# Kernel optimization log

Hardware: AMD Instinct MI355X
Metric: run time of the kernel (lower is better)

Reference implementation:

```python
import jax, jax.numpy as jnp
import numpy as np

BLOCK_SIZE = 256
N_EMBD = 384
HEAD_SIZE = 384
B = 256
T = 256


def setup_inputs() -> dict:
    key = jax.random.key(0)
    kx, kk, kq, kv = jax.random.split(key, 4)
    scale = 1.0 / np.sqrt(N_EMBD)
    x = jax.random.normal(kx, (B, T, N_EMBD), dtype=jnp.float32)
    Wk = jax.random.normal(kk, (HEAD_SIZE, N_EMBD), dtype=jnp.float32) * scale
    Wq = jax.random.normal(kq, (HEAD_SIZE, N_EMBD), dtype=jnp.float32) * scale
    Wv = jax.random.normal(kv, (HEAD_SIZE, N_EMBD), dtype=jnp.float32) * scale
    return {"x": x, "Wk": Wk, "Wq": Wq, "Wv": Wv}


def reference(x, Wk, Wq, Wv):
    # Single-head causal self-attention; equals forward_with_cache at prefill
    # (fresh cache, cache_index=0, T tokens) and forward_no_cache.
    # Linear layers are bias-free: y = x @ W.T
    k = jnp.einsum('btc,hc->bth', x, Wk)  # [B,T,H]
    q = jnp.einsum('btc,hc->bth', x, Wq)
    v = jnp.einsum('btc,hc->bth', x, Wv)
    inv_sqrt_hs = jnp.asarray(HEAD_SIZE, x.dtype) ** -0.5
    wei = jnp.einsum('bth,bsh->bts', q, k) * inv_sqrt_hs  # [B,T,T]
    causal = jnp.tril(jnp.ones((T, T), dtype=bool))
    wei = jnp.where(causal, wei, jnp.asarray(-jnp.inf, wei.dtype))
    wei = jax.nn.softmax(wei, axis=-1)
    # dropout is identity in eval mode
    out = jnp.einsum('bts,bsh->bth', wei, v)  # [B,T,H]
    return out
```

## Files before the change

### kernel.cpp

```cpp
#include <hip/hip_runtime.h>

#define B_ 256
#define T_ 256
#define C_ 384
#define H_ 384

typedef float f4 __attribute__((ext_vector_type(4)));
typedef float f32x4 __attribute__((ext_vector_type(4)));
typedef short bf8 __attribute__((ext_vector_type(8)));
typedef short s8v __attribute__((ext_vector_type(8)));
typedef short s4v __attribute__((ext_vector_type(4)));

__device__ __forceinline__ short f2bf(float f) {
  unsigned u = __builtin_bit_cast(unsigned, f);
  u += 0x7FFFu + ((u >> 16) & 1u);
  return (short)(u >> 16);
}

__device__ __forceinline__ void gload_lds16(const void* g, void* l) {
  __builtin_amdgcn_global_load_lds(
      (const __attribute__((address_space(1))) unsigned int*)g,
      (__attribute__((address_space(3))) unsigned int*)l, 16, 0, 0);
}

__global__ __launch_bounds__(256) void convert_kernel(
    const float* __restrict__ x, const float* __restrict__ wk,
    const float* __restrict__ wq, const float* __restrict__ wv,
    short* __restrict__ xb, short* __restrict__ wb) {
  const int NXG = (B_ * T_ * C_) / 8;
  const int NWG = (H_ * C_) / 8;
  const int total = NXG + 3 * NWG;
  for (int g = blockIdx.x * 256 + threadIdx.x; g < total; g += gridDim.x * 256) {
    const float* src;
    short* dst;
    if (g < NXG) {
      src = x + (size_t)g * 8;
      dst = xb + (size_t)g * 8;
    } else {
      int h = g - NXG;
      int wsel = h / NWG;
      int o = h - wsel * NWG;
      const float* wp = wsel == 0 ? wk : (wsel == 1 ? wq : wv);
      src = wp + (size_t)o * 8;
      dst = wb + (size_t)wsel * (H_ * C_) + (size_t)o * 8;
    }
    f4 f0 = *(const f4*)src;
    f4 f1 = *(const f4*)(src + 4);
    s8v r;
    r[0] = f2bf(f0[0]); r[1] = f2bf(f0[1]); r[2] = f2bf(f0[2]); r[3] = f2bf(f0[3]);
    r[4] = f2bf(f1[0]); r[5] = f2bf(f1[1]); r[6] = f2bf(f1[2]); r[7] = f2bf(f1[3]);
    *(s8v*)dst = r;
  }
}

__global__ __launch_bounds__(512, 2) void proj_gemm(
    const short* __restrict__ xb, const short* __restrict__ wb,
    short* __restrict__ kb, short* __restrict__ qbuf, short* __restrict__ vt) {
  __shared__ __align__(16) short lA[2][512 * 64];
  __shared__ __align__(16) short lB[2][128 * 64];
  const int tid = threadIdx.x;
  const int bid = blockIdx.x;
  const int swz = (bid & 7) * 144 + (bid >> 3);
  const int nb = swz % 9;
  const int mb = swz / 9;
  const int m0 = mb * 512, gn0 = nb * 128;
  const int w = tid >> 6, l = tid & 63;
  const int wrm = w >> 1, wcn = w & 1;

  auto STAGE = [&](int buf, int t) {
    const int k0 = t * 64;
#pragma unroll
    for (int j = 0; j < 8; ++j) {
      const int flat = j * 512 + tid;
      const int row = flat >> 3;
      const int colg = ((flat & 7) ^ (row & 7)) * 8;
      gload_lds16(xb + (size_t)(m0 + row) * C_ + k0 + colg,
                  (char*)&lA[buf][0] + flat * 16);
    }
#pragma unroll
    for (int j = 0; j < 2; ++j) {
      const int flat = j * 512 + tid;
      const int row = flat >> 3;
      const int colg = ((flat & 7) ^ (row & 7)) * 8;
      gload_lds16(wb + (size_t)(gn0 + row) * C_ + k0 + colg,
                  (char*)&lB[buf][0] + flat * 16);
    }
  };

  f32x4 acc[8][4] = {};
  STAGE(0, 0);
#pragma unroll
  for (int t = 0; t < 6; ++t) {
    const int cur = t & 1;
    if (t < 5) {
      STAGE(cur ^ 1, t + 1);
      asm volatile("s_waitcnt vmcnt(10)" ::: "memory");
    } else {
      asm volatile("s_waitcnt vmcnt(0)" ::: "memory");
    }
    __builtin_amdgcn_s_barrier();
    __builtin_amdgcn_sched_barrier(0);
    const short* A = &lA[cur][0];
    const short* Bt = &lB[cur][0];
#pragma unroll
    for (int ks = 0; ks < 2; ++ks) {
      const int kg = ks * 4 + (l >> 4);
      bf8 av[8], bv[4];
#pragma unroll
      for (int mt = 0; mt < 8; ++mt) {
        const int ra = wrm * 128 + mt * 16 + (l & 15);
        av[mt] = *(const bf8*)&A[ra * 64 + ((kg ^ (ra & 7)) << 3)];
      }
#pragma unroll
      for (int nt = 0; nt < 4; ++nt) {
        const int rb = wcn * 64 + nt * 16 + (l & 15);
        bv[nt] = *(const bf8*)&Bt[rb * 64 + ((kg ^ (rb & 7)) << 3)];
      }
      __builtin_amdgcn_s_setprio(1);
#pragma unroll
      for (int mt = 0; mt < 8; ++mt)
#pragma unroll
        for (int nt = 0; nt < 4; ++nt)
          acc[mt][nt] = __builtin_amdgcn_mfma_f32_16x16x32_bf16(
              av[mt], bv[nt], acc[mt][nt], 0, 0, 0);
      __builtin_amdgcn_s_setprio(0);
    }
    __builtin_amdgcn_sched_barrier(0);
    __builtin_amdgcn_s_barrier();
  }
  const int proj = nb / 3;
  const int gcb = (nb % 3) * 128 + wcn * 64 + (l & 15);
  const int tok0 = m0 + wrm * 128 + ((l >> 4) * 4);
  if (proj < 2) {
    short* dst = proj == 0 ? kb : qbuf;
#pragma unroll
    for (int mt = 0; mt < 8; ++mt)
#pragma unroll
      for (int nt = 0; nt < 4; ++nt)
#pragma unroll
        for (int r = 0; r < 4; ++r)
          dst[(size_t)(tok0 + mt * 16 + r) * H_ + gcb + nt * 16] =
              f2bf(acc[mt][nt][r]);
  } else {
    const int bb = tok0 >> 8;
    const int tl0 = tok0 & 255;
#pragma unroll
    for (int mt = 0; mt < 8; ++mt)
#pragma unroll
      for (int nt = 0; nt < 4; ++nt) {
        s4v pk;
        pk[0] = f2bf(acc[mt][nt][0]); pk[1] = f2bf(acc[mt][nt][1]);
        pk[2] = f2bf(acc[mt][nt][2]); pk[3] = f2bf(acc[mt][nt][3]);
        *(s4v*)&vt[(size_t)bb * (H_ * T_) + (size_t)(gcb + nt * 16) * T_ +
                   tl0 + mt * 16] = pk;
      }
  }
}

__global__ __launch_bounds__(256, 2) void attn_kernel(
    const short* __restrict__ qbuf, const short* __restrict__ kb,
    const short* __restrict__ vt, float* __restrict__ out) {
  __shared__ __align__(16) short Kl[2][256 * 64];
  short* Pl = &Kl[0][0];
  const int bid = blockIdx.x;
  const int swzb = (bid & 7) * 128 + (bid >> 3);
  const int b = swzb >> 2;
  const int qi = swzb & 3;
  const int t0 = qi * 64;
  const int SKV = t0 + 64;
  const int ntile = SKV >> 4;
  const int nks = SKV >> 5;
  const int tid = threadIdx.x;
  const int w = tid >> 6, l = tid & 63;

  bf8 qv[6][2];
  {
    const short* qrow =
        qbuf + (size_t)(b * T_ + t0 + w * 16 + (l & 15)) * H_ + (l >> 4) * 8;
#pragma unroll
    for (int hc = 0; hc < 6; ++hc)
#pragma unroll
      for (int ks = 0; ks < 2; ++ks)
        qv[hc][ks] = *(const bf8*)(qrow + hc * 64 + ks * 32);
  }

  auto STAGE = [&](int buf, int hc) {
    const int h0 = hc * 64;
#pragma unroll
    for (int j = 0; j < 8; ++j) {
      const int flat = j * 256 + tid;
      const int row = flat >> 3;
      const int colg = ((flat & 7) ^ (row & 7)) * 8;
      gload_lds16(kb + (size_t)(b * T_ + row) * H_ + h0 + colg,
                  (char*)&Kl[buf][0] + flat * 16);
    }
  };

  f32x4 sa[16] = {};
  STAGE(0, 0);
#pragma unroll
  for (int hc = 0; hc < 6; ++hc) {
    if (hc < 5) {
      STAGE((hc + 1) & 1, hc + 1);
      asm volatile("s_waitcnt vmcnt(8)" ::: "memory");
    } else {
      asm volatile("s_waitcnt vmcnt(0)" ::: "memory");
    }
    __builtin_amdgcn_s_barrier();
    __builtin_amdgcn_sched_barrier(0);
    const short* Kb = &Kl[hc & 1][0];
#pragma unroll
    for (int ks = 0; ks < 2; ++ks) {
      const int kg = ks * 4 + (l >> 4);
      __builtin_amdgcn_s_setprio(1);
#pragma unroll
      for (int nt = 0; nt < 16; ++nt)
        if (nt < ntile) {
          const int rk = nt * 16 + (l & 15);
          bf8 bv = *(const bf8*)&Kb[rk * 64 + ((kg ^ (rk & 7)) << 3)];
          sa[nt] = __builtin_amdgcn_mfma_f32_16x16x32_bf16(qv[hc][ks], bv,
                                                           sa[nt], 0, 0, 0);
        }
      __builtin_amdgcn_s_setprio(0);
    }
    __builtin_amdgcn_sched_barrier(0);
    __builtin_amdgcn_s_barrier();
  }

  const float scale = 0.05103103630798287f;
  const int rbl = w * 16 + (l >> 4) * 4;
#pragma unroll
  for (int r = 0; r < 4; ++r) {
    const int prow = rbl + r;
    const int trow = t0 + prow;
    float vv[16];
    float m = -3.0e38f;
#pragma unroll
    for (int nt = 0; nt < 16; ++nt)
      if (nt < ntile) {
        const int col = nt * 16 + (l & 15);
        float v = sa[nt][r] * scale;
        if (col > trow) v = -3.0e38f;
        vv[nt] = v;
        m = fmaxf(m, v);
      }
    m = fmaxf(m, __shfl_xor(m, 1));
    m = fmaxf(m, __shfl_xor(m, 2));
    m = fmaxf(m, __shfl_xor(m, 4));
    m = fmaxf(m, __shfl_xor(m, 8));
    float s = 0.f;
#pragma unroll
    for (int nt = 0; nt < 16; ++nt)
      if (nt < ntile) {
        vv[nt] = __expf(vv[nt] - m);
        s += vv[nt];
      }
    s += __shfl_xor(s, 1);
    s += __shfl_xor(s, 2);
    s += __shfl_xor(s, 4);
    s += __shfl_xor(s, 8);
    const float inv = 1.0f / s;
    const int sw = (prow & 7) << 3;
#pragma unroll
    for (int nt = 0; nt < 16; ++nt)
      if (nt < ntile) {
        const int col = nt * 16 + (l & 15);
        Pl[prow * 256 + (col ^ sw)] = f2bf(vv[nt] * inv);
      }
  }
  __syncthreads();

  const size_t vbase = (size_t)b * (H_ * T_);
  bf8 vc[6], vn[6];
  {
    const int kk0 = (l >> 4) * 8;
#pragma unroll
    for (int nt = 0; nt < 6; ++nt)
      vc[nt] = *(const bf8*)&vt[vbase + (size_t)(w * 96 + nt * 16 + (l & 15)) * T_ + kk0];
  }
  f32x4 o[4][6] = {};
  for (int ks = 0; ks < nks; ++ks) {
    const int kk = ks * 32 + (l >> 4) * 8;
    if (ks + 1 < nks) {
      const int kk2 = kk + 32;
#pragma unroll
      for (int nt = 0; nt < 6; ++nt)
        vn[nt] = *(const bf8*)&vt[vbase + (size_t)(w * 96 + nt * 16 + (l & 15)) * T_ + kk2];
    }
    bf8 av[4];
#pragma unroll
    for (int mt = 0; mt < 4; ++mt) {
      const int rp = mt * 16 + (l & 15);
      av[mt] = *(const bf8*)&Pl[rp * 256 + (kk ^ ((rp & 7) << 3))];
    }
    __builtin_amdgcn_s_setprio(1);
#pragma unroll
    for (int nt = 0; nt < 6; ++nt)
#pragma unroll
      for (int mt = 0; mt < 4; ++mt)
        o[mt][nt] = __builtin_amdgcn_mfma_f32_16x16x32_bf16(av[mt], vc[nt],
                                                            o[mt][nt], 0, 0, 0);
    __builtin_amdgcn_s_setprio(0);
#pragma unroll
    for (int nt = 0; nt < 6; ++nt) vc[nt] = vn[nt];
  }
#pragma unroll
  for (int mt = 0; mt < 4; ++mt) {
    const int tok = b * T_ + t0 + mt * 16 + (l >> 4) * 4;
#pragma unroll
    for (int nt = 0; nt < 6; ++nt) {
      const int d = w * 96 + nt * 16 + (l & 15);
#pragma unroll
      for (int r = 0; r < 4; ++r)
        out[(size_t)(tok + r) * H_ + d] = o[mt][nt][r];
    }
  }
}

extern "C" void kernel_launch(void* const* d_in, const int* in_sizes, int n_in,
                              void* d_out, int out_size, void* d_ws, size_t ws_size,
                              hipStream_t stream) {
  (void)in_sizes; (void)n_in; (void)out_size; (void)ws_size;
  const float* x = (const float*)d_in[0];
  const float* wk = (const float*)d_in[1];
  const float* wq = (const float*)d_in[2];
  const float* wv = (const float*)d_in[3];
  float* out = (float*)d_out;
  char* ws = (char*)d_ws;
  const size_t SZ = (size_t)B_ * T_ * H_ * 2;
  short* kbuf = (short*)ws;
  short* qbuf = (short*)(ws + SZ);
  short* vt   = (short*)(ws + 2 * SZ);
  short* xb = (short*)d_out;
  short* wb = (short*)((char*)d_out + SZ);
  convert_kernel<<<2048, 256, 0, stream>>>(x, wk, wq, wv, xb, wb);
  proj_gemm<<<1152, 512, 0, stream>>>(xb, wb, kbuf, qbuf, vt);
  attn_kernel<<<1024, 256, 0, stream>>>(qbuf, kbuf, vt, out);
}
```

Baseline: 326.2 us.

## Fuse fp32-to-bf16 conversion into projection GEMM tile loading

Drops the separate convert kernel. The projection GEMM now reads fp32 x and weights straight from global memory into registers, packs them to bf16 with v_cvt_pk_bf16_f32, and writes them into LDS. This removes a full write and re-read of a bf16 copy of x plus one kernel launch. In exchange it gives up async global_load_lds in favour of register staging, which raises register pressure, and each of the 9 N-blocks rereads fp32 x, doubling the bytes per reread.

```diff
diff --git a/kernel.cpp b/kernel.cpp
--- a/kernel.cpp
+++ b/kernel.cpp
@@ -8,8 +8,8 @@
 typedef float f4 __attribute__((ext_vector_type(4)));
 typedef float f32x4 __attribute__((ext_vector_type(4)));
 typedef short bf8 __attribute__((ext_vector_type(8)));
-typedef short s8v __attribute__((ext_vector_type(8)));
 typedef short s4v __attribute__((ext_vector_type(4)));
+typedef unsigned int u4v __attribute__((ext_vector_type(4)));
 
 __device__ __forceinline__ short f2bf(float f) {
   unsigned u = __builtin_bit_cast(unsigned, f);
@@ -17,44 +17,30 @@
   return (short)(u >> 16);
 }
 
+__device__ __forceinline__ unsigned cvtpk(float a, float b) {
+  unsigned r;
+  asm("v_cvt_pk_bf16_f32 %0, %1, %2" : "=v"(r) : "v"(a), "v"(b));
+  return r;
+}
+
+__device__ __forceinline__ u4v pack8(f4 lo, f4 hi) {
+  u4v r;
+  r[0] = cvtpk(lo[0], lo[1]);
+  r[1] = cvtpk(lo[2], lo[3]);
+  r[2] = cvtpk(hi[0], hi[1]);
+  r[3] = cvtpk(hi[2], hi[3]);
+  return r;
+}
+
 __device__ __forceinline__ void gload_lds16(const void* g, void* l) {
   __builtin_amdgcn_global_load_lds(
       (const __attribute__((address_space(1))) unsigned int*)g,
       (__attribute__((address_space(3))) unsigned int*)l, 16, 0, 0);
 }
 
-__global__ __launch_bounds__(256) void convert_kernel(
+__global__ __launch_bounds__(512, 2) void proj_gemm(
     const float* __restrict__ x, const float* __restrict__ wk,
     const float* __restrict__ wq, const float* __restrict__ wv,
-    short* __restrict__ xb, short* __restrict__ wb) {
-  const int NXG = (B_ * T_ * C_) / 8;
-  const int NWG = (H_ * C_) / 8;
-  const int total = NXG + 3 * NWG;
-  for (int g = blockIdx.x * 256 + threadIdx.x; g < total; g += gridDim.x * 256) {
-    const float* src;
-    short* dst;
-    if (g < NXG) {
-      src = x + (size_t)g * 8;
-      dst = xb + (size_t)g * 8;
-    } else {
-      int h = g - NXG;
-      int wsel = h / NWG;
-      int o = h - wsel * NWG;
-      const float* wp = wsel == 0 ? wk : (wsel == 1 ? wq : wv);
-      src = wp + (size_t)o * 8;
-      dst = wb + (size_t)wsel * (H_ * C_) + (size_t)o * 8;
-    }
-    f4 f0 = *(const f4*)src;
-    f4 f1 = *(const f4*)(src + 4);
-    s8v r;
-    r[0] = f2bf(f0[0]); r[1] = f2bf(f0[1]); r[2] = f2bf(f0[2]); r[3] = f2bf(f0[3]);
-    r[4] = f2bf(f1[0]); r[5] = f2bf(f1[1]); r[6] = f2bf(f1[2]); r[7] = f2bf(f1[3]);
-    *(s8v*)dst = r;
-  }
-}
-
-__global__ __launch_bounds__(512, 2) void proj_gemm(
-    const short* __restrict__ xb, const short* __restrict__ wb,
     short* __restrict__ kb, short* __restrict__ qbuf, short* __restrict__ vt) {
   __shared__ __align__(16) short lA[2][512 * 64];
   __shared__ __align__(16) short lB[2][128 * 64];
@@ -63,43 +49,60 @@
   const int swz = (bid & 7) * 144 + (bid >> 3);
   const int nb = swz % 9;
   const int mb = swz / 9;
-  const int m0 = mb * 512, gn0 = nb * 128;
+  const int m0 = mb * 512;
   const int w = tid >> 6, l = tid & 63;
   const int wrm = w >> 1, wcn = w & 1;
-
-  auto STAGE = [&](int buf, int t) {
+  const int proj = nb / 3;
+  const float* Wp = proj == 0 ? wk : (proj == 1 ? wq : wv);
+  const int wrow0 = (nb % 3) * 128;
+
+  f4 ar[8][2];
+  f4 br[2][2];
+
+  auto LOADT = [&](int t) {
     const int k0 = t * 64;
 #pragma unroll
     for (int j = 0; j < 8; ++j) {
       const int flat = j * 512 + tid;
       const int row = flat >> 3;
-      const int colg = ((flat & 7) ^ (row & 7)) * 8;
-      gload_lds16(xb + (size_t)(m0 + row) * C_ + k0 + colg,
-                  (char*)&lA[buf][0] + flat * 16);
+      const int cg = ((flat & 7) ^ (row & 7)) * 8;
+      const float* p = x + (size_t)(m0 + row) * C_ + k0 + cg;
+      ar[j][0] = *(const f4*)p;
+      ar[j][1] = *(const f4*)(p + 4);
     }
 #pragma unroll
     for (int j = 0; j < 2; ++j) {
       const int flat = j * 512 + tid;
       const int row = flat >> 3;
-      const int colg = ((flat & 7) ^ (row & 7)) * 8;
-      gload_lds16(wb + (size_t)(gn0 + row) * C_ + k0 + colg,
-                  (char*)&lB[buf][0] + flat * 16);
+      const int cg = ((flat & 7) ^ (row & 7)) * 8;
+      const float* p = Wp + (size_t)(wrow0 + row) * C_ + k0 + cg;
+      br[j][0] = *(const f4*)p;
+      br[j][1] = *(const f4*)(p + 4);
     }
   };
+  auto WRITET = [&](int buf) {
+#pragma unroll
+    for (int j = 0; j < 8; ++j) {
+      const int flat = j * 512 + tid;
+      *(u4v*)((char*)&lA[buf][0] + flat * 16) = pack8(ar[j][0], ar[j][1]);
+    }
+#pragma unroll
+    for (int j = 0; j < 2; ++j) {
+      const int flat = j * 512 + tid;
+      *(u4v*)((char*)&lB[buf][0] + flat * 16) = pack8(br[j][0], br[j][1]);
+    }
+  };
 
   f32x4 acc[8][4] = {};
-  STAGE(0, 0);
+  LOADT(0);
+  WRITET(0);
+  asm volatile("s_waitcnt lgkmcnt(0)" ::: "memory");
+  __builtin_amdgcn_s_barrier();
+  __builtin_amdgcn_sched_barrier(0);
 #pragma unroll
   for (int t = 0; t < 6; ++t) {
     const int cur = t & 1;
-    if (t < 5) {
-      STAGE(cur ^ 1, t + 1);
-      asm volatile("s_waitcnt vmcnt(10)" ::: "memory");
-    } else {
-      asm volatile("s_waitcnt vmcnt(0)" ::: "memory");
-    }
-    __builtin_amdgcn_s_barrier();
-    __builtin_amdgcn_sched_barrier(0);
+    if (t < 5) LOADT(t + 1);
     const short* A = &lA[cur][0];
     const short* Bt = &lB[cur][0];
 #pragma unroll
@@ -125,10 +128,12 @@
               av[mt], bv[nt], acc[mt][nt], 0, 0, 0);
       __builtin_amdgcn_s_setprio(0);
     }
+    if (t < 5) WRITET(cur ^ 1);
+    asm volatile("s_waitcnt lgkmcnt(0)" ::: "memory");
     __builtin_amdgcn_sched_barrier(0);
     __builtin_amdgcn_s_barrier();
-  }
-  const int proj = nb / 3;
+    __builtin_amdgcn_sched_barrier(0);
+  }
   const int gcb = (nb % 3) * 128 + wcn * 64 + (l & 15);
   const int tok0 = m0 + wrm * 128 + ((l >> 4) * 4);
   if (proj < 2) {
@@ -331,9 +336,6 @@
   short* kbuf = (short*)ws;
   short* qbuf = (short*)(ws + SZ);
   short* vt   = (short*)(ws + 2 * SZ);
-  short* xb = (short*)d_out;
-  short* wb = (short*)((char*)d_out + SZ);
-  convert_kernel<<<2048, 256, 0, stream>>>(x, wk, wq, wv, xb, wb);
-  proj_gemm<<<1152, 512, 0, stream>>>(xb, wb, kbuf, qbuf, vt);
+  proj_gemm<<<1152, 512, 0, stream>>>(x, wk, wq, wv, kbuf, qbuf, vt);
   attn_kernel<<<1024, 256, 0, stream>>>(qbuf, kbuf, vt, out);
 }
```

Result: slower. 610.0 us (+87.0%).

## Keep weight tile resident in LDS and stream four 128-row A tiles per block

Applied to the files above, without the earlier changes.

The projection GEMM now loads the block's full 128x384 weight slice into LDS once and keeps it there. It then streams four consecutive 128-row x tiles through a 4-deep LDS ring buffer, writing each output tile as soon as its K loop finishes. Blocks shrink to 256 threads with smaller per-wave accumulators and one block per CU, which removes repeated weight loads. The cost is lower occupancy, a large LDS footprint, and epilogue stores that now sit inside the main loop.

```diff
diff --git a/kernel.cpp b/kernel.cpp
--- a/kernel.cpp
+++ b/kernel.cpp
@@ -53,72 +53,72 @@
   }
 }
 
-__global__ __launch_bounds__(512, 2) void proj_gemm(
+__global__ __launch_bounds__(256, 1) void proj_gemm(
     const short* __restrict__ xb, const short* __restrict__ wb,
     short* __restrict__ kb, short* __restrict__ qbuf, short* __restrict__ vt) {
-  __shared__ __align__(16) short lA[2][512 * 64];
-  __shared__ __align__(16) short lB[2][128 * 64];
+  __shared__ __align__(16) short Bres[128 * 384];
+  __shared__ __align__(16) short Abuf[4][128 * 64];
   const int tid = threadIdx.x;
   const int bid = blockIdx.x;
   const int swz = (bid & 7) * 144 + (bid >> 3);
   const int nb = swz % 9;
-  const int mb = swz / 9;
-  const int m0 = mb * 512, gn0 = nb * 128;
+  const int mg = swz / 9;
+  const int gn0 = nb * 128;
   const int w = tid >> 6, l = tid & 63;
-  const int wrm = w >> 1, wcn = w & 1;
-
-  auto STAGE = [&](int buf, int t) {
-    const int k0 = t * 64;
-#pragma unroll
-    for (int j = 0; j < 8; ++j) {
-      const int flat = j * 512 + tid;
-      const int row = flat >> 3;
-      const int colg = ((flat & 7) ^ (row & 7)) * 8;
-      gload_lds16(xb + (size_t)(m0 + row) * C_ + k0 + colg,
-                  (char*)&lA[buf][0] + flat * 16);
-    }
-#pragma unroll
-    for (int j = 0; j < 2; ++j) {
-      const int flat = j * 512 + tid;
-      const int row = flat >> 3;
-      const int colg = ((flat & 7) ^ (row & 7)) * 8;
-      gload_lds16(wb + (size_t)(gn0 + row) * C_ + k0 + colg,
-                  (char*)&lB[buf][0] + flat * 16);
+  const int wr = w >> 1, wc = w & 1;
+
+#pragma unroll
+  for (int j = 0; j < 24; ++j) {
+    const int flat = j * 256 + tid;
+    const int row = flat / 48;
+    const int g = flat % 48;
+    const int kc = g >> 3, sub = g & 7;
+    const int colg = kc * 64 + ((sub ^ (row & 7)) << 3);
+    gload_lds16(wb + (size_t)(gn0 + row) * C_ + colg, (char*)Bres + flat * 16);
+  }
+  auto SA = [&](int i) {
+    const int m0 = (mg * 4 + i / 6) * 128;
+    const int k0 = (i % 6) * 64;
+    char* dst = (char*)&Abuf[i & 3][0];
+#pragma unroll
+    for (int j = 0; j < 4; ++j) {
+      const int flat = j * 256 + tid;
+      const int row = flat >> 3, sub = flat & 7;
+      const int colg = (sub ^ (row & 7)) << 3;
+      gload_lds16(xb + (size_t)(m0 + row) * C_ + k0 + colg, dst + flat * 16);
     }
   };
 
-  f32x4 acc[8][4] = {};
-  STAGE(0, 0);
-#pragma unroll
-  for (int t = 0; t < 6; ++t) {
-    const int cur = t & 1;
-    if (t < 5) {
-      STAGE(cur ^ 1, t + 1);
-      asm volatile("s_waitcnt vmcnt(10)" ::: "memory");
-    } else {
-      asm volatile("s_waitcnt vmcnt(0)" ::: "memory");
-    }
+  SA(0); SA(1); SA(2);
+  f32x4 acc[4][4] = {};
+#pragma unroll
+  for (int i = 0; i < 24; ++i) {
+    if (i + 3 < 24) SA(i + 3);
+    if (i <= 20)      asm volatile("s_waitcnt vmcnt(12)" ::: "memory");
+    else if (i == 21) asm volatile("s_waitcnt vmcnt(8)" ::: "memory");
+    else if (i == 22) asm volatile("s_waitcnt vmcnt(4)" ::: "memory");
+    else              asm volatile("s_waitcnt vmcnt(0)" ::: "memory");
     __builtin_amdgcn_s_barrier();
     __builtin_amdgcn_sched_barrier(0);
-    const short* A = &lA[cur][0];
-    const short* Bt = &lB[cur][0];
+    const short* A = &Abuf[i & 3][0];
+    const int t = i % 6;
 #pragma unroll
     for (int ks = 0; ks < 2; ++ks) {
       const int kg = ks * 4 + (l >> 4);
-      bf8 av[8], bv[4];
-#pragma unroll
-      for (int mt = 0; mt < 8; ++mt) {
-        const int ra = wrm * 128 + mt * 16 + (l & 15);
+      bf8 av[4], bv[4];
+#pragma unroll
+      for (int mt = 0; mt < 4; ++mt) {
+        const int ra = wr * 64 + mt * 16 + (l & 15);
         av[mt] = *(const bf8*)&A[ra * 64 + ((kg ^ (ra & 7)) << 3)];
       }
 #pragma unroll
       for (int nt = 0; nt < 4; ++nt) {
-        const int rb = wcn * 64 + nt * 16 + (l & 15);
-        bv[nt] = *(const bf8*)&Bt[rb * 64 + ((kg ^ (rb & 7)) << 3)];
+        const int rb = wc * 64 + nt * 16 + (l & 15);
+        bv[nt] = *(const bf8*)&Bres[rb * 384 + t * 64 + ((kg ^ (rb & 7)) << 3)];
       }
       __builtin_amdgcn_s_setprio(1);
 #pragma unroll
-      for (int mt = 0; mt < 8; ++mt)
+      for (int mt = 0; mt < 4; ++mt)
 #pragma unroll
         for (int nt = 0; nt < 4; ++nt)
           acc[mt][nt] = __builtin_amdgcn_mfma_f32_16x16x32_bf16(
@@ -127,33 +127,41 @@
     }
     __builtin_amdgcn_sched_barrier(0);
     __builtin_amdgcn_s_barrier();
-  }
-  const int proj = nb / 3;
-  const int gcb = (nb % 3) * 128 + wcn * 64 + (l & 15);
-  const int tok0 = m0 + wrm * 128 + ((l >> 4) * 4);
-  if (proj < 2) {
-    short* dst = proj == 0 ? kb : qbuf;
-#pragma unroll
-    for (int mt = 0; mt < 8; ++mt)
-#pragma unroll
-      for (int nt = 0; nt < 4; ++nt)
-#pragma unroll
-        for (int r = 0; r < 4; ++r)
-          dst[(size_t)(tok0 + mt * 16 + r) * H_ + gcb + nt * 16] =
-              f2bf(acc[mt][nt][r]);
-  } else {
-    const int bb = tok0 >> 8;
-    const int tl0 = tok0 & 255;
-#pragma unroll
-    for (int mt = 0; mt < 8; ++mt)
-#pragma unroll
-      for (int nt = 0; nt < 4; ++nt) {
-        s4v pk;
-        pk[0] = f2bf(acc[mt][nt][0]); pk[1] = f2bf(acc[mt][nt][1]);
-        pk[2] = f2bf(acc[mt][nt][2]); pk[3] = f2bf(acc[mt][nt][3]);
-        *(s4v*)&vt[(size_t)bb * (H_ * T_) + (size_t)(gcb + nt * 16) * T_ +
-                   tl0 + mt * 16] = pk;
-      }
+    if (t == 5) {
+      const int m0 = (mg * 4 + i / 6) * 128;
+      const int proj = nb / 3;
+      const int gcb = (nb % 3) * 128 + wc * 64 + (l & 15);
+      const int tok0 = m0 + wr * 64 + ((l >> 4) * 4);
+      if (proj < 2) {
+        short* dst = proj == 0 ? kb : qbuf;
+#pragma unroll
+        for (int mt = 0; mt < 4; ++mt)
+#pragma unroll
+          for (int nt = 0; nt < 4; ++nt)
+#pragma unroll
+            for (int r = 0; r < 4; ++r)
+              dst[(size_t)(tok0 + mt * 16 + r) * H_ + gcb + nt * 16] =
+                  f2bf(acc[mt][nt][r]);
+      } else {
+        const int bb = tok0 >> 8;
+        const int tl0 = tok0 & 255;
+#pragma unroll
+        for (int mt = 0; mt < 4; ++mt)
+#pragma unroll
+          for (int nt = 0; nt < 4; ++nt) {
+            s4v pk;
+            pk[0] = f2bf(acc[mt][nt][0]); pk[1] = f2bf(acc[mt][nt][1]);
+            pk[2] = f2bf(acc[mt][nt][2]); pk[3] = f2bf(acc[mt][nt][3]);
+            *(s4v*)&vt[(size_t)bb * (H_ * T_) + (size_t)(gcb + nt * 16) * T_ +
+                       tl0 + mt * 16] = pk;
+          }
+      }
+#pragma unroll
+      for (int mt = 0; mt < 4; ++mt)
+#pragma unroll
+        for (int nt = 0; nt < 4; ++nt)
+          acc[mt][nt] = (f32x4){0.f, 0.f, 0.f, 0.f};
+    }
   }
 }
 
@@ -334,6 +342,6 @@
   short* xb = (short*)d_out;
   short* wb = (short*)((char*)d_out + SZ);
   convert_kernel<<<2048, 256, 0, stream>>>(x, wk, wq, wv, xb, wb);
-  proj_gemm<<<1152, 512, 0, stream>>>(xb, wb, kbuf, qbuf, vt);
+  proj_gemm<<<1152, 256, 0, stream>>>(xb, wb, kbuf, qbuf, vt);
   attn_kernel<<<1024, 256, 0, stream>>>(qbuf, kbuf, vt, out);
 }
```

New measurement: 339.7 us. 1.04x slower.
